# Performance work log

Hardware: AMD Instinct MI355X
Metric: run time of the kernel (lower is better)

Reference implementation:

```python
import jax, jax.numpy as jnp
import numpy as np

B, T, F, H, C = 128, 2048, 2, 64, 2
EPS = 1e-5  # BatchNorm eps (eval mode, running stats)


def setup_inputs() -> dict:
    key = jax.random.key(0)
    ks = jax.random.split(key, 23)
    rn = lambda k, s, sc=0.1: jax.random.normal(k, s, jnp.float32) * sc
    return {
        "x": jax.random.normal(ks[0], (B, T, F), jnp.float32),
        "tags": jax.random.randint(ks[1], (B, T), 0, C),
        "cw1": rn(ks[2], (H, F)), "cb1": rn(ks[3], (H,)),
        "cwr": rn(ks[4], (3, H, H)), "cbr": rn(ks[5], (3, H)),
        "bn_g": 1.0 + rn(ks[6], (4, H)), "bn_b": rn(ks[7], (4, H)),
        "bn_m": rn(ks[8], (4, H)),
        "bn_v": 0.5 + jax.random.uniform(ks[9], (4, H), jnp.float32),
        "wih_f": rn(ks[10], (4 * H, H)), "whh_f": rn(ks[11], (4 * H, H)),
        "bih_f": rn(ks[12], (4 * H,)), "bhh_f": rn(ks[13], (4 * H,)),
        "wih_b": rn(ks[14], (4 * H, H)), "whh_b": rn(ks[15], (4 * H, H)),
        "bih_b": rn(ks[16], (4 * H,)), "bhh_b": rn(ks[17], (4 * H,)),
        "fc_w": rn(ks[18], (C, 2 * H)), "fc_b": rn(ks[19], (C,)),
        "crf_start": rn(ks[20], (C,)), "crf_end": rn(ks[21], (C,)),
        "crf_trans": rn(ks[22], (C, C)),
    }


def _block(y, w, b, g, be, m, v):
    # Conv1d(kernel_size=1) == per-timestep linear; GELU (exact erf); eval BatchNorm1d
    y = jnp.einsum('bti,hi->bth', y, w) + b
    y = jax.nn.gelu(y, approximate=False)
    return (y - m) / jnp.sqrt(v + EPS) * g + be


def _lstm(xs, wih, whh, bih, bhh):
    # xs: [T, B, H]; PyTorch gate order i, f, g, o
    h0 = jnp.zeros((xs.shape[1], whh.shape[1]), xs.dtype)

    def step(carry, xt):
        h, c = carry
        z = xt @ wih.T + h @ whh.T + bih + bhh
        i, f, g, o = jnp.split(z, 4, axis=-1)
        c = jax.nn.sigmoid(f) * c + jax.nn.sigmoid(i) * jnp.tanh(g)
        h = jax.nn.sigmoid(o) * jnp.tanh(c)
        return (h, c), h

    _, hs = jax.lax.scan(step, (h0, h0), xs)
    return hs  # [T, B, H]


def reference(x, tags, cw1, cb1, cwr, cbr, bn_g, bn_b, bn_m, bn_v,
              wih_f, whh_f, bih_f, bhh_f, wih_b, whh_b, bih_b, bhh_b,
              fc_w, fc_b, crf_start, crf_end, crf_trans):
    # --- 1x1-conv stack (dropout is identity in eval) ---
    y = _block(x, cw1, cb1, bn_g[0], bn_b[0], bn_m[0], bn_v[0])
    for i in range(3):
        y = _block(y, cwr[i], cbr[i], bn_g[i + 1], bn_b[i + 1], bn_m[i + 1], bn_v[i + 1])
    # --- BiLSTM ---
    xt = jnp.transpose(y, (1, 0, 2))                       # [T, B, H]
    hf = _lstm(xt, wih_f, whh_f, bih_f, bhh_f)
    hb = _lstm(xt[::-1], wih_b, whh_b, bih_b, bhh_b)[::-1]
    h = jnp.concatenate([hf, hb], axis=-1)                 # [T, B, 2H]
    em = jnp.transpose(h @ fc_w.T + fc_b, (1, 0, 2))       # [B, T, C] emissions
    # --- CRF log-partition (forward algorithm, lax.scan over time) ---
    alpha0 = crf_start + em[:, 0]                          # [B, C]

    def step(alpha, et):
        a = jax.scipy.special.logsumexp(alpha[:, :, None] + crf_trans[None], axis=1) + et
        return a, None

    alpha, _ = jax.lax.scan(step, alpha0, jnp.transpose(em[:, 1:], (1, 0, 2)))
    logZ = jax.scipy.special.logsumexp(alpha + crf_end, axis=1)  # [B]
    # --- gold-path score ---
    num = crf_start[tags[:, 0]] + crf_end[tags[:, -1]]
    num = num + jnp.take_along_axis(em, tags[:, :, None], axis=2)[..., 0].sum(axis=1)
    num = num + crf_trans[tags[:, :-1], tags[:, 1:]].sum(axis=1)
    # model returns -crf(logits, tags) with reduction='sum' -> scalar NLL
    return -(num - logZ).sum()
```

## Files before the change

### kernel.cpp

```cpp
#include <hip/hip_runtime.h>
#include <hip/hip_bf16.h>

#define BB 128
#define TT 2048
#define HH 64
#define BT (BB * TT)
#define EPS_BN 1e-5f

typedef unsigned short ushort_t;
typedef short s8v __attribute__((ext_vector_type(8)));
typedef float f4v __attribute__((ext_vector_type(4)));

__device__ __forceinline__ float gelu_exact(float x) {
    return 0.5f * x * (1.0f + erff(x * 0.70710678118654752440f));
}
__device__ __forceinline__ ushort_t f2bf(float v) {
    __hip_bfloat16 h = __float2bfloat16(v);
    return *reinterpret_cast<ushort_t*>(&h);
}
__device__ __forceinline__ float lse2(float a, float b) {
    float m = fmaxf(a, b);
    return m + log1pf(__expf(-fabsf(a - b)));
}

__global__ __launch_bounds__(256, 4) void conv_kernel(
    const float* __restrict__ x, const float* __restrict__ cw1, const float* __restrict__ cb1,
    const float* __restrict__ cwr, const float* __restrict__ cbr,
    const float* __restrict__ bn_g, const float* __restrict__ bn_b,
    const float* __restrict__ bn_m, const float* __restrict__ bn_v,
    ushort_t* __restrict__ y) {
    __shared__ ushort_t s_wc[3 * 64 * 64];
    __shared__ float s_l1[64 * 4];
    __shared__ float s_sc[256], s_sh[256];
    __shared__ float s_cb[192];
    __shared__ ushort_t s_act[4][1024];

    int tid = threadIdx.x;
    for (int i = tid; i < 3 * 64 * 64; i += 256) {
        int row = (i >> 6) & 63, col = i & 63;
        unsigned by = (unsigned)((i >> 6) * 128 + col * 2) ^ (unsigned)((row & 7) << 4);
        s_wc[by >> 1] = f2bf(cwr[i]);
    }
    if (tid < 64) {
        s_l1[tid * 4 + 0] = cw1[tid * 2 + 0];
        s_l1[tid * 4 + 1] = cw1[tid * 2 + 1];
        s_l1[tid * 4 + 2] = cb1[tid];
    }
    if (tid < 256) {
        float sc = bn_g[tid] * rsqrtf(bn_v[tid] + EPS_BN);
        s_sc[tid] = sc;
        s_sh[tid] = bn_b[tid] - bn_m[tid] * sc;
    }
    if (tid < 192) s_cb[tid] = cbr[tid];
    __syncthreads();

    int wid = tid >> 6, l = tid & 63;
    int lrow = l & 15, lgrp = l >> 4;
    ushort_t* act = s_act[wid];
    int gwave = blockIdx.x * 4 + wid;

    for (int strip = gwave; strip < 16384; strip += 4096) {
        int p0 = strip << 4;
        float2 xv = ((const float2*)x)[p0 + lrow];
        s8v fa0, fa1;
#pragma unroll
        for (int j = 0; j < 8; ++j) {
            int c0 = lgrp * 8 + j, c1 = 32 + c0;
            float t0 = s_l1[c0 * 4] * xv.x + s_l1[c0 * 4 + 1] * xv.y + s_l1[c0 * 4 + 2];
            t0 = gelu_exact(t0) * s_sc[c0] + s_sh[c0];
            fa0[j] = (short)f2bf(t0);
            float t1 = s_l1[c1 * 4] * xv.x + s_l1[c1 * 4 + 1] * xv.y + s_l1[c1 * 4 + 2];
            t1 = gelu_exact(t1) * s_sc[c1] + s_sh[c1];
            fa1[j] = (short)f2bf(t1);
        }
#pragma unroll
        for (int L = 0; L < 3; ++L) {
            f4v acc[4];
#pragma unroll
            for (int nt = 0; nt < 4; ++nt) {
                acc[nt] = (f4v){0.f, 0.f, 0.f, 0.f};
                int row = nt * 16 + lrow;
                unsigned b0 = (unsigned)(L * 8192 + row * 128 + lgrp * 16) ^ (unsigned)((row & 7) << 4);
                unsigned b1 = (unsigned)(L * 8192 + row * 128 + lgrp * 16 + 64) ^ (unsigned)((row & 7) << 4);
                s8v fb0 = *(const s8v*)((const char*)s_wc + b0);
                s8v fb1 = *(const s8v*)((const char*)s_wc + b1);
                acc[nt] = __builtin_amdgcn_mfma_f32_16x16x32_bf16(fa0, fb0, acc[nt], 0, 0, 0);
                acc[nt] = __builtin_amdgcn_mfma_f32_16x16x32_bf16(fa1, fb1, acc[nt], 0, 0, 0);
            }
#pragma unroll
            for (int nt = 0; nt < 4; ++nt) {
                int ch = nt * 16 + lrow;
#pragma unroll
                for (int i = 0; i < 4; ++i) {
                    float v = acc[nt][i] + s_cb[L * 64 + ch];
                    v = gelu_exact(v) * s_sc[(L + 1) * 64 + ch] + s_sh[(L + 1) * 64 + ch];
                    int pos = lgrp * 4 + i;
                    unsigned by = (unsigned)(pos * 128 + ch * 2) ^ (unsigned)((pos & 7) << 4);
                    *(ushort_t*)((char*)act + by) = f2bf(v);
                }
            }
            if (L < 2) {
                unsigned r0 = (unsigned)(lrow * 128 + lgrp * 16) ^ (unsigned)((lrow & 7) << 4);
                unsigned r1 = (unsigned)(lrow * 128 + lgrp * 16 + 64) ^ (unsigned)((lrow & 7) << 4);
                fa0 = *(const s8v*)((const char*)act + r0);
                fa1 = *(const s8v*)((const char*)act + r1);
            }
        }
        int prow = l >> 2, pc = l & 3;
        unsigned so0 = (unsigned)(prow * 128 + pc * 32) ^ (unsigned)((prow & 7) << 4);
        unsigned so1 = (unsigned)(prow * 128 + pc * 32 + 16) ^ (unsigned)((prow & 7) << 4);
        s8v v0 = *(const s8v*)((const char*)act + so0);
        s8v v1 = *(const s8v*)((const char*)act + so1);
        char* yb = (char*)y + (size_t)(p0 + prow) * 128 + pc * 32;
        *(s8v*)yb = v0;
        *(s8v*)(yb + 16) = v1;
    }
}

__device__ __forceinline__ void em_emit(const float (*hist)[64], s8v femB0, s8v femB1,
                                        int lrow, int lgrp, float* __restrict__ em_ws,
                                        int dir, int b, int t_base, int dstep) {
    s8v fa0, fa1;
#pragma unroll
    for (int jj = 0; jj < 8; ++jj) {
        fa0[jj] = (short)f2bf(hist[lrow][lgrp * 8 + jj]);
        fa1[jj] = (short)f2bf(hist[lrow][32 + lgrp * 8 + jj]);
    }
    f4v acc = (f4v){0.f, 0.f, 0.f, 0.f};
    acc = __builtin_amdgcn_mfma_f32_16x16x32_bf16(fa0, femB0, acc, 0, 0, 0);
    acc = __builtin_amdgcn_mfma_f32_16x16x32_bf16(fa1, femB1, acc, 0, 0, 0);
    if (lrow < 2) {
#pragma unroll
        for (int i = 0; i < 4; ++i) {
            int s_loc = lgrp * 4 + i;
            int t = t_base + dstep * s_loc;
            em_ws[(((size_t)dir * TT + t) * BB + b) * 2 + lrow] = acc[i];
        }
    }
}

#define DOT4(g) (h0.x*wq[g][0].x + h0.y*wq[g][0].y + h0.z*wq[g][0].z + h0.w*wq[g][0].w \
               + h1.x*wq[g][1].x + h1.y*wq[g][1].y + h1.z*wq[g][1].z + h1.w*wq[g][1].w \
               + h2.x*wq[g][2].x + h2.y*wq[g][2].y + h2.z*wq[g][2].z + h2.w*wq[g][2].w \
               + h3.x*wq[g][3].x + h3.y*wq[g][3].y + h3.z*wq[g][3].z + h3.w*wq[g][3].w)

__global__ __launch_bounds__(256, 1) void lstm_kernel(
    const ushort_t* __restrict__ y,
    const float* __restrict__ whh_f, const float* __restrict__ whh_b,
    const float* __restrict__ wih_f, const float* __restrict__ wih_b,
    const float* __restrict__ bih_f, const float* __restrict__ bhh_f,
    const float* __restrict__ bih_b, const float* __restrict__ bhh_b,
    const float* __restrict__ fc_w, float* __restrict__ em_ws) {
    int blk = blockIdx.x;
    int dir = blk >> 7;
    int b = blk & 127;
    const float* whh = dir ? whh_b : whh_f;
    const float* wih = dir ? wih_b : wih_f;
    const float* bih = dir ? bih_b : bih_f;
    const float* bhh = dir ? bhh_b : bhh_f;

    int tid = threadIdx.x;
    int u = tid >> 2, kq = tid & 3;
    int wid = tid >> 6, l = tid & 63;
    int lrow = l & 15, lgrp = l >> 4;

    __shared__ ushort_t s_wih[256 * 64];
    __shared__ float s_pb[256];
    __shared__ float zbuf[16][256];
    __shared__ ushort_t s_y[16 * 64];
    __shared__ float hist[16][64];

    for (int i = tid; i < 256 * 64; i += 256) {
        int row = i >> 6, col = i & 63;
        unsigned by = (unsigned)(row * 128 + col * 2) ^ (unsigned)((row & 7) << 4);
        s_wih[by >> 1] = f2bf(wih[i]);
    }
    s_pb[tid] = bih[tid] + bhh[tid];
    if (tid < 64) hist[15][tid] = 0.f;

    float4 wq[4][4];
#pragma unroll
    for (int g = 0; g < 4; ++g)
#pragma unroll
        for (int m = 0; m < 4; ++m)
            wq[g][m] = *(const float4*)(whh + (size_t)(g * 64 + u) * 64 + kq * 16 + m * 4);

    s8v femB0 = {0, 0, 0, 0, 0, 0, 0, 0}, femB1 = {0, 0, 0, 0, 0, 0, 0, 0};
    if (wid == 0 && lrow < 2) {
#pragma unroll
        for (int jj = 0; jj < 8; ++jj) {
            int u0 = lgrp * 8 + jj;
            femB0[jj] = (short)f2bf(fc_w[lrow * 128 + dir * 64 + u0]);
            femB1[jj] = (short)f2bf(fc_w[lrow * 128 + dir * 64 + 32 + u0]);
        }
    }

    int t0 = dir ? (TT - 1) : 0;
    int dstep = dir ? -1 : 1;
    int m_st = tid >> 4, ch4 = tid & 15;
    const char* ybase = (const char*)y + (size_t)b * TT * 128;
    unsigned sy_by = (unsigned)(m_st * 128 + ch4 * 8) ^ (unsigned)((m_st & 7) << 4);
    uint2 yreg = *(const uint2*)(ybase + (size_t)(t0 + dstep * m_st) * 128 + ch4 * 8);

    __syncthreads();

    float c = 0.f;
    for (int strip = 0; strip < 128; ++strip) {
        *(uint2*)((char*)s_y + sy_by) = yreg;
        __syncthreads();
        {
            s8v fa0 = *(const s8v*)((const char*)s_y +
                        ((unsigned)(lrow * 128 + lgrp * 16) ^ (unsigned)((lrow & 7) << 4)));
            s8v fa1 = *(const s8v*)((const char*)s_y +
                        ((unsigned)(lrow * 128 + lgrp * 16 + 64) ^ (unsigned)((lrow & 7) << 4)));
#pragma unroll
            for (int nt = 0; nt < 4; ++nt) {
                int row = wid * 64 + nt * 16 + lrow;
                s8v fb0 = *(const s8v*)((const char*)s_wih +
                            ((unsigned)(row * 128 + lgrp * 16) ^ (unsigned)((row & 7) << 4)));
                s8v fb1 = *(const s8v*)((const char*)s_wih +
                            ((unsigned)(row * 128 + lgrp * 16 + 64) ^ (unsigned)((row & 7) << 4)));
                f4v acc = (f4v){0.f, 0.f, 0.f, 0.f};
                acc = __builtin_amdgcn_mfma_f32_16x16x32_bf16(fa0, fb0, acc, 0, 0, 0);
                acc = __builtin_amdgcn_mfma_f32_16x16x32_bf16(fa1, fb1, acc, 0, 0, 0);
                int u_ = nt * 16 + lrow;
                float bias = s_pb[row];
#pragma unroll
                for (int i = 0; i < 4; ++i) {
                    int pos = lgrp * 4 + i;
                    zbuf[pos][(u_ * 4 + wid) ^ lgrp] = acc[i] + bias;
                }
            }
            if (strip > 0 && wid == 0)
                em_emit(hist, femB0, femB1, lrow, lgrp, em_ws, dir, b,
                        t0 + dstep * ((strip - 1) * 16), dstep);
        }
        __syncthreads();
        float z_reg[16];
#pragma unroll
        for (int j = 0; j < 16; ++j) z_reg[j] = zbuf[j][tid ^ ((j >> 2) & 3)];
        if (strip + 1 < 128) {
            int tn = t0 + dstep * ((strip + 1) * 16 + m_st);
            yreg = *(const uint2*)(ybase + (size_t)tn * 128 + ch4 * 8);
        }
#pragma unroll
        for (int j = 0; j < 16; ++j) {
            int jm1 = (j + 15) & 15;
            const float4* hb4 = (const float4*)&hist[jm1][kq * 16];
            float4 h0 = hb4[0], h1 = hb4[1], h2 = hb4[2], h3 = hb4[3];
            float a0 = DOT4(0), a1 = DOT4(1), a2 = DOT4(2), a3 = DOT4(3);
            float zr = z_reg[j];
            a0 += (kq == 0) ? zr : 0.f;
            a1 += (kq == 1) ? zr : 0.f;
            a2 += (kq == 2) ? zr : 0.f;
            a3 += (kq == 3) ? zr : 0.f;
            a0 += __shfl_xor(a0, 1); a0 += __shfl_xor(a0, 2);
            a1 += __shfl_xor(a1, 1); a1 += __shfl_xor(a1, 2);
            a2 += __shfl_xor(a2, 1); a2 += __shfl_xor(a2, 2);
            a3 += __shfl_xor(a3, 1); a3 += __shfl_xor(a3, 2);
            float zg = (kq == 0) ? a0 : (kq == 1) ? a1 : (kq == 2) ? a2 : a3;
            float sgm = 1.f / (1.f + __expf((kq == 2) ? (-zg - zg) : -zg));
            float val = (kq == 2) ? (2.f * sgm - 1.f) : sgm;
            float v1 = __shfl_xor(val, 1), v2 = __shfl_xor(val, 2), v3 = __shfl_xor(val, 3);
            float gi = (kq == 0) ? val : (kq == 1) ? v1 : (kq == 2) ? v2 : v3;
            float gf = (kq == 1) ? val : (kq == 0) ? v1 : (kq == 3) ? v2 : v3;
            float gg = (kq == 2) ? val : (kq == 3) ? v1 : (kq == 0) ? v2 : v3;
            float go = (kq == 3) ? val : (kq == 2) ? v1 : (kq == 1) ? v2 : v3;
            c = gf * c + gi * gg;
            float e2 = __expf(2.f * c);
            float h = go * (1.f - 2.f / (e2 + 1.f));
            if (kq == 0) hist[j][u] = h;
            __syncthreads();
        }
    }
    if (wid == 0)
        em_emit(hist, femB0, femB1, lrow, lgrp, em_ws, dir, b,
                t0 + dstep * (127 * 16), dstep);
}

__global__ __launch_bounds__(128) void crf_kernel(
    const float* __restrict__ em_ws, const int* __restrict__ tags,
    const float* __restrict__ fc_b, const float* __restrict__ crf_start,
    const float* __restrict__ crf_end, const float* __restrict__ crf_trans,
    float* __restrict__ out) {
    int b = threadIdx.x;
    float fb0 = fc_b[0], fb1 = fc_b[1];
    float t00 = crf_trans[0], t01 = crf_trans[1], t10 = crf_trans[2], t11 = crf_trans[3];
    float s0 = crf_start[0], s1 = crf_start[1];
    float ee0 = crf_end[0], ee1 = crf_end[1];
    const float2* p0 = (const float2*)em_ws;
    const float2* p1 = p0 + (size_t)TT * BB;
    const int* tgp = tags + (size_t)b * TT;

    float2 ea = p0[b];
    float2 eb = p1[b];
    float e0 = ea.x + eb.x + fb0;
    float e1 = ea.y + eb.y + fb1;
    float a0 = s0 + e0, a1 = s1 + e1;
    int tp = tgp[0];
    float num = (tp ? s1 : s0) + (tp ? e1 : e0);

    int t = 1;
    for (; t + 8 <= TT; t += 8) {
        float2 ca[8], cb[8];
        int ct[8];
#pragma unroll
        for (int i = 0; i < 8; ++i) {
            ca[i] = p0[(size_t)(t + i) * BB + b];
            cb[i] = p1[(size_t)(t + i) * BB + b];
            ct[i] = tgp[t + i];
        }
#pragma unroll
        for (int i = 0; i < 8; ++i) {
            float f0 = ca[i].x + cb[i].x + fb0;
            float f1 = ca[i].y + cb[i].y + fb1;
            float n0 = lse2(a0 + t00, a1 + t10) + f0;
            float n1 = lse2(a0 + t01, a1 + t11) + f1;
            a0 = n0; a1 = n1;
            int tgi = ct[i];
            num += (tgi ? f1 : f0) + (tp ? (tgi ? t11 : t10) : (tgi ? t01 : t00));
            tp = tgi;
        }
    }
    for (; t < TT; ++t) {
        float2 ca = p0[(size_t)t * BB + b];
        float2 cb = p1[(size_t)t * BB + b];
        float f0 = ca.x + cb.x + fb0;
        float f1 = ca.y + cb.y + fb1;
        float n0 = lse2(a0 + t00, a1 + t10) + f0;
        float n1 = lse2(a0 + t01, a1 + t11) + f1;
        a0 = n0; a1 = n1;
        int tgi = tgp[t];
        num += (tgi ? f1 : f0) + (tp ? (tgi ? t11 : t10) : (tgi ? t01 : t00));
        tp = tgi;
    }
    num += tp ? ee1 : ee0;
    float logZ = lse2(a0 + ee0, a1 + ee1);
    float nll = logZ - num;
    __shared__ float red[BB];
    red[b] = nll;
    __syncthreads();
    if (b == 0) {
        float s = 0.f;
        for (int i = 0; i < BB; ++i) s += red[i];
        out[0] = s;
    }
}

extern "C" void kernel_launch(void* const* d_in, const int* in_sizes, int n_in,
                              void* d_out, int out_size, void* d_ws, size_t ws_size,
                              hipStream_t stream) {
    const float* x = (const float*)d_in[0];
    const int* tags = (const int*)d_in[1];
    const float* cw1 = (const float*)d_in[2];
    const float* cb1 = (const float*)d_in[3];
    const float* cwr = (const float*)d_in[4];
    const float* cbr = (const float*)d_in[5];
    const float* bn_g = (const float*)d_in[6];
    const float* bn_b = (const float*)d_in[7];
    const float* bn_m = (const float*)d_in[8];
    const float* bn_v = (const float*)d_in[9];
    const float* wih_f = (const float*)d_in[10];
    const float* whh_f = (const float*)d_in[11];
    const float* bih_f = (const float*)d_in[12];
    const float* bhh_f = (const float*)d_in[13];
    const float* wih_b = (const float*)d_in[14];
    const float* whh_b = (const float*)d_in[15];
    const float* bih_b = (const float*)d_in[16];
    const float* bhh_b = (const float*)d_in[17];
    const float* fc_w = (const float*)d_in[18];
    const float* fc_b = (const float*)d_in[19];
    const float* crf_start = (const float*)d_in[20];
    const float* crf_end = (const float*)d_in[21];
    const float* crf_trans = (const float*)d_in[22];
    float* out = (float*)d_out;

    ushort_t* y = (ushort_t*)d_ws;
    float* em = (float*)((char*)d_ws + (size_t)BT * 64 * 2);

    conv_kernel<<<1024, 256, 0, stream>>>(x, cw1, cb1, cwr, cbr, bn_g, bn_b, bn_m, bn_v, y);
    lstm_kernel<<<256, 256, 0, stream>>>(y, whh_f, whh_b, wih_f, wih_b,
                                         bih_f, bhh_f, bih_b, bhh_b, fc_w, em);
    crf_kernel<<<1, 128, 0, stream>>>(em, tags, fc_b, crf_start, crf_end, crf_trans, out);
}
```

Baseline: 2.232 ms.

## Batch LSTM recurrence over 16 sequences with MFMA and parallelize CRF over time

The LSTM moves from one block per (direction, batch) with scalar FP32 dot products to 16 blocks that each handle 16 batch rows. Both the recurrent h@Whh and the input projections now run as bf16 MFMA, with weights held in registers and h kept in a swizzled LDS ring. The CRF forward pass switches from one thread per batch scanning all 2048 steps to a time-parallel scheme: each thread builds a 2x2 log-semiring transfer product over 16 steps, and the products are then combined, with a separate sum kernel at the end. The trade-offs are fewer blocks (16 of the GPU's many CUs), bf16 rounding of h in the recurrence, and one extra kernel launch.

```diff
diff --git a/kernel.cpp b/kernel.cpp
--- a/kernel.cpp
+++ b/kernel.cpp
@@ -117,32 +117,87 @@
     }
 }
 
-__device__ __forceinline__ void em_emit(const float (*hist)[64], s8v femB0, s8v femB1,
-                                        int lrow, int lgrp, float* __restrict__ em_ws,
-                                        int dir, int b, int t_base, int dstep) {
-    s8v fa0, fa1;
-#pragma unroll
-    for (int jj = 0; jj < 8; ++jj) {
-        fa0[jj] = (short)f2bf(hist[lrow][lgrp * 8 + jj]);
-        fa1[jj] = (short)f2bf(hist[lrow][32 + lgrp * 8 + jj]);
-    }
-    f4v acc = (f4v){0.f, 0.f, 0.f, 0.f};
-    acc = __builtin_amdgcn_mfma_f32_16x16x32_bf16(fa0, femB0, acc, 0, 0, 0);
-    acc = __builtin_amdgcn_mfma_f32_16x16x32_bf16(fa1, femB1, acc, 0, 0, 0);
-    if (lrow < 2) {
+__device__ __forceinline__ unsigned ring_addr(int slot, int bb, int ub) {
+    return (unsigned)(slot * 2048) + (((unsigned)(bb * 128 + ub)) ^ ((unsigned)((bb & 7) << 4)));
+}
+
+template <int PAR>
+__device__ __forceinline__ void lstm_strip(
+    int s, int w, int lb, int lg, int b, int d, int t0, int dstep,
+    const s8v (&whhA)[4][2], const s8v (&wihA)[4][2],
+    const f4v (&zbias)[4], const s8v (&femA)[2],
+    const s8v (&ybCur)[4][2], s8v (&ybNxt)[4][2],
+    float (&cst)[4], ushort_t* ring,
+    const char* __restrict__ ybase, float2* __restrict__ emv) {
+    f4v zin[4][4];
+#pragma unroll
+    for (int g = 0; g < 4; ++g)
+#pragma unroll
+        for (int ct = 0; ct < 4; ++ct) {
+            f4v a = zbias[g];
+            a = __builtin_amdgcn_mfma_f32_16x16x32_bf16(wihA[g][0], ybCur[ct][0], a, 0, 0, 0);
+            a = __builtin_amdgcn_mfma_f32_16x16x32_bf16(wihA[g][1], ybCur[ct][1], a, 0, 0, 0);
+            zin[g][ct] = a;
+        }
+    if (s + 1 < 512) {
+#pragma unroll
+        for (int ct = 0; ct < 4; ++ct) {
+            int t = t0 + dstep * ((s + 1) * 4 + ct);
+            const char* p = ybase + (size_t)t * 128 + lg * 16;
+            ybNxt[ct][0] = *(const s8v*)p;
+            ybNxt[ct][1] = *(const s8v*)(p + 64);
+        }
+    }
+    if (w == 0 && s > 0) {
+#pragma unroll
+        for (int ct = 0; ct < 4; ++ct) {
+            int slot = (1 - PAR) * 4 + ct;
+            s8v hlo = *(const s8v*)((const char*)ring + ring_addr(slot, lb, lg * 16));
+            s8v hhi = *(const s8v*)((const char*)ring + ring_addr(slot, lb, 64 + lg * 16));
+            f4v a = (f4v){0.f, 0.f, 0.f, 0.f};
+            a = __builtin_amdgcn_mfma_f32_16x16x32_bf16(femA[0], hlo, a, 0, 0, 0);
+            a = __builtin_amdgcn_mfma_f32_16x16x32_bf16(femA[1], hhi, a, 0, 0, 0);
+            if (lg == 0) {
+                int t = t0 + dstep * ((s - 1) * 4 + ct);
+                emv[((size_t)d * TT + t) * BB + b] = make_float2(a[0], a[1]);
+            }
+        }
+    }
+#pragma unroll
+    for (int j = 0; j < 4; ++j) {
+        const int prev = (j == 0) ? ((1 - PAR) * 4 + 3) : (PAR * 4 + j - 1);
+        const int slot = PAR * 4 + j;
+        s8v hlo = *(const s8v*)((const char*)ring + ring_addr(prev, lb, lg * 16));
+        s8v hhi = *(const s8v*)((const char*)ring + ring_addr(prev, lb, 64 + lg * 16));
+        f4v a0 = __builtin_amdgcn_mfma_f32_16x16x32_bf16(whhA[0][0], hlo, zin[0][j], 0, 0, 0);
+        f4v a1 = __builtin_amdgcn_mfma_f32_16x16x32_bf16(whhA[1][0], hlo, zin[1][j], 0, 0, 0);
+        f4v a2 = __builtin_amdgcn_mfma_f32_16x16x32_bf16(whhA[2][0], hlo, zin[2][j], 0, 0, 0);
+        f4v a3 = __builtin_amdgcn_mfma_f32_16x16x32_bf16(whhA[3][0], hlo, zin[3][j], 0, 0, 0);
+        a0 = __builtin_amdgcn_mfma_f32_16x16x32_bf16(whhA[0][1], hhi, a0, 0, 0, 0);
+        a1 = __builtin_amdgcn_mfma_f32_16x16x32_bf16(whhA[1][1], hhi, a1, 0, 0, 0);
+        a2 = __builtin_amdgcn_mfma_f32_16x16x32_bf16(whhA[2][1], hhi, a2, 0, 0, 0);
+        a3 = __builtin_amdgcn_mfma_f32_16x16x32_bf16(whhA[3][1], hhi, a3, 0, 0, 0);
+        unsigned hp0 = 0, hp1 = 0;
 #pragma unroll
         for (int i = 0; i < 4; ++i) {
-            int s_loc = lgrp * 4 + i;
-            int t = t_base + dstep * s_loc;
-            em_ws[(((size_t)dir * TT + t) * BB + b) * 2 + lrow] = acc[i];
-        }
-    }
-}
-
-#define DOT4(g) (h0.x*wq[g][0].x + h0.y*wq[g][0].y + h0.z*wq[g][0].z + h0.w*wq[g][0].w \
-               + h1.x*wq[g][1].x + h1.y*wq[g][1].y + h1.z*wq[g][1].z + h1.w*wq[g][1].w \
-               + h2.x*wq[g][2].x + h2.y*wq[g][2].y + h2.z*wq[g][2].z + h2.w*wq[g][2].w \
-               + h3.x*wq[g][3].x + h3.y*wq[g][3].y + h3.z*wq[g][3].z + h3.w*wq[g][3].w)
+            float zi = a0[i], zf = a1[i], zg = a2[i], zo = a3[i];
+            float ig = 1.f / (1.f + __expf(-zi));
+            float fg = 1.f / (1.f + __expf(-zf));
+            float gg = 1.f - 2.f / (__expf(2.f * zg) + 1.f);
+            float og = 1.f / (1.f + __expf(-zo));
+            float cn = fg * cst[i] + ig * gg;
+            cst[i] = cn;
+            float th = 1.f - 2.f / (__expf(2.f * cn) + 1.f);
+            unsigned hb_ = (unsigned)f2bf(og * th);
+            if (i == 0) hp0 = hb_;
+            else if (i == 1) hp0 |= hb_ << 16;
+            else if (i == 2) hp1 = hb_;
+            else hp1 |= hb_ << 16;
+        }
+        *(uint2*)((char*)ring + ring_addr(slot, lb, (16 * w + lg * 4) * 2)) = make_uint2(hp0, hp1);
+        __syncthreads();
+    }
+}
 
 __global__ __launch_bounds__(256, 1) void lstm_kernel(
     const ushort_t* __restrict__ y,
@@ -151,196 +206,155 @@
     const float* __restrict__ bih_f, const float* __restrict__ bhh_f,
     const float* __restrict__ bih_b, const float* __restrict__ bhh_b,
     const float* __restrict__ fc_w, float* __restrict__ em_ws) {
-    int blk = blockIdx.x;
-    int dir = blk >> 7;
-    int b = blk & 127;
-    const float* whh = dir ? whh_b : whh_f;
-    const float* wih = dir ? wih_b : wih_f;
-    const float* bih = dir ? bih_b : bih_f;
-    const float* bhh = dir ? bhh_b : bhh_f;
-
+    __shared__ ushort_t ring[8 * 1024];
+    int d = blockIdx.x >> 3, bg = blockIdx.x & 7;
+    const float* whh = d ? whh_b : whh_f;
+    const float* wih = d ? wih_b : wih_f;
+    const float* bih = d ? bih_b : bih_f;
+    const float* bhh = d ? bhh_b : bhh_f;
     int tid = threadIdx.x;
-    int u = tid >> 2, kq = tid & 3;
-    int wid = tid >> 6, l = tid & 63;
-    int lrow = l & 15, lgrp = l >> 4;
-
-    __shared__ ushort_t s_wih[256 * 64];
-    __shared__ float s_pb[256];
-    __shared__ float zbuf[16][256];
-    __shared__ ushort_t s_y[16 * 64];
-    __shared__ float hist[16][64];
-
-    for (int i = tid; i < 256 * 64; i += 256) {
-        int row = i >> 6, col = i & 63;
-        unsigned by = (unsigned)(row * 128 + col * 2) ^ (unsigned)((row & 7) << 4);
-        s_wih[by >> 1] = f2bf(wih[i]);
-    }
-    s_pb[tid] = bih[tid] + bhh[tid];
-    if (tid < 64) hist[15][tid] = 0.f;
-
-    float4 wq[4][4];
+    int w = tid >> 6, l = tid & 63, lb = l & 15, lg = l >> 4;
+    int b = bg * 16 + lb;
+
+    for (int i = tid; i < 4096; i += 256) ((unsigned*)ring)[i] = 0u;
+
+    s8v whhA[4][2], wihA[4][2];
 #pragma unroll
     for (int g = 0; g < 4; ++g)
 #pragma unroll
-        for (int m = 0; m < 4; ++m)
-            wq[g][m] = *(const float4*)(whh + (size_t)(g * 64 + u) * 64 + kq * 16 + m * 4);
-
-    s8v femB0 = {0, 0, 0, 0, 0, 0, 0, 0}, femB1 = {0, 0, 0, 0, 0, 0, 0, 0};
-    if (wid == 0 && lrow < 2) {
-#pragma unroll
-        for (int jj = 0; jj < 8; ++jj) {
-            int u0 = lgrp * 8 + jj;
-            femB0[jj] = (short)f2bf(fc_w[lrow * 128 + dir * 64 + u0]);
-            femB1[jj] = (short)f2bf(fc_w[lrow * 128 + dir * 64 + 32 + u0]);
-        }
-    }
-
-    int t0 = dir ? (TT - 1) : 0;
-    int dstep = dir ? -1 : 1;
-    int m_st = tid >> 4, ch4 = tid & 15;
+        for (int kh = 0; kh < 2; ++kh) {
+            s8v va, vb;
+#pragma unroll
+            for (int j = 0; j < 8; ++j) {
+                int row = g * 64 + 16 * w + lb;
+                int k = kh * 32 + lg * 8 + j;
+                va[j] = (short)f2bf(whh[(size_t)row * 64 + k]);
+                vb[j] = (short)f2bf(wih[(size_t)row * 64 + k]);
+            }
+            whhA[g][kh] = va;
+            wihA[g][kh] = vb;
+        }
+    f4v zbias[4];
+#pragma unroll
+    for (int g = 0; g < 4; ++g)
+#pragma unroll
+        for (int i = 0; i < 4; ++i) {
+            int u = 16 * w + lg * 4 + i;
+            zbias[g][i] = bih[g * 64 + u] + bhh[g * 64 + u];
+        }
+    s8v femA[2];
+#pragma unroll
+    for (int kh = 0; kh < 2; ++kh)
+#pragma unroll
+        for (int j = 0; j < 8; ++j) {
+            int k = kh * 32 + lg * 8 + j;
+            femA[kh][j] = (lb < 2) ? (short)f2bf(fc_w[lb * 128 + d * 64 + k]) : (short)0;
+        }
+
+    int t0 = d ? (TT - 1) : 0;
+    int dstep = d ? -1 : 1;
     const char* ybase = (const char*)y + (size_t)b * TT * 128;
-    unsigned sy_by = (unsigned)(m_st * 128 + ch4 * 8) ^ (unsigned)((m_st & 7) << 4);
-    uint2 yreg = *(const uint2*)(ybase + (size_t)(t0 + dstep * m_st) * 128 + ch4 * 8);
-
+    float2* emv = (float2*)em_ws;
+
+    s8v ybA[4][2], ybB[4][2];
+#pragma unroll
+    for (int ct = 0; ct < 4; ++ct) {
+        int t = t0 + dstep * ct;
+        const char* p = ybase + (size_t)t * 128 + lg * 16;
+        ybA[ct][0] = *(const s8v*)p;
+        ybA[ct][1] = *(const s8v*)(p + 64);
+    }
+    float cst[4] = {0.f, 0.f, 0.f, 0.f};
     __syncthreads();
 
-    float c = 0.f;
-    for (int strip = 0; strip < 128; ++strip) {
-        *(uint2*)((char*)s_y + sy_by) = yreg;
-        __syncthreads();
-        {
-            s8v fa0 = *(const s8v*)((const char*)s_y +
-                        ((unsigned)(lrow * 128 + lgrp * 16) ^ (unsigned)((lrow & 7) << 4)));
-            s8v fa1 = *(const s8v*)((const char*)s_y +
-                        ((unsigned)(lrow * 128 + lgrp * 16 + 64) ^ (unsigned)((lrow & 7) << 4)));
-#pragma unroll
-            for (int nt = 0; nt < 4; ++nt) {
-                int row = wid * 64 + nt * 16 + lrow;
-                s8v fb0 = *(const s8v*)((const char*)s_wih +
-                            ((unsigned)(row * 128 + lgrp * 16) ^ (unsigned)((row & 7) << 4)));
-                s8v fb1 = *(const s8v*)((const char*)s_wih +
-                            ((unsigned)(row * 128 + lgrp * 16 + 64) ^ (unsigned)((row & 7) << 4)));
-                f4v acc = (f4v){0.f, 0.f, 0.f, 0.f};
-                acc = __builtin_amdgcn_mfma_f32_16x16x32_bf16(fa0, fb0, acc, 0, 0, 0);
-                acc = __builtin_amdgcn_mfma_f32_16x16x32_bf16(fa1, fb1, acc, 0, 0, 0);
-                int u_ = nt * 16 + lrow;
-                float bias = s_pb[row];
-#pragma unroll
-                for (int i = 0; i < 4; ++i) {
-                    int pos = lgrp * 4 + i;
-                    zbuf[pos][(u_ * 4 + wid) ^ lgrp] = acc[i] + bias;
-                }
-            }
-            if (strip > 0 && wid == 0)
-                em_emit(hist, femB0, femB1, lrow, lgrp, em_ws, dir, b,
-                        t0 + dstep * ((strip - 1) * 16), dstep);
-        }
-        __syncthreads();
-        float z_reg[16];
-#pragma unroll
-        for (int j = 0; j < 16; ++j) z_reg[j] = zbuf[j][tid ^ ((j >> 2) & 3)];
-        if (strip + 1 < 128) {
-            int tn = t0 + dstep * ((strip + 1) * 16 + m_st);
-            yreg = *(const uint2*)(ybase + (size_t)tn * 128 + ch4 * 8);
-        }
-#pragma unroll
-        for (int j = 0; j < 16; ++j) {
-            int jm1 = (j + 15) & 15;
-            const float4* hb4 = (const float4*)&hist[jm1][kq * 16];
-            float4 h0 = hb4[0], h1 = hb4[1], h2 = hb4[2], h3 = hb4[3];
-            float a0 = DOT4(0), a1 = DOT4(1), a2 = DOT4(2), a3 = DOT4(3);
-            float zr = z_reg[j];
-            a0 += (kq == 0) ? zr : 0.f;
-            a1 += (kq == 1) ? zr : 0.f;
-            a2 += (kq == 2) ? zr : 0.f;
-            a3 += (kq == 3) ? zr : 0.f;
-            a0 += __shfl_xor(a0, 1); a0 += __shfl_xor(a0, 2);
-            a1 += __shfl_xor(a1, 1); a1 += __shfl_xor(a1, 2);
-            a2 += __shfl_xor(a2, 1); a2 += __shfl_xor(a2, 2);
-            a3 += __shfl_xor(a3, 1); a3 += __shfl_xor(a3, 2);
-            float zg = (kq == 0) ? a0 : (kq == 1) ? a1 : (kq == 2) ? a2 : a3;
-            float sgm = 1.f / (1.f + __expf((kq == 2) ? (-zg - zg) : -zg));
-            float val = (kq == 2) ? (2.f * sgm - 1.f) : sgm;
-            float v1 = __shfl_xor(val, 1), v2 = __shfl_xor(val, 2), v3 = __shfl_xor(val, 3);
-            float gi = (kq == 0) ? val : (kq == 1) ? v1 : (kq == 2) ? v2 : v3;
-            float gf = (kq == 1) ? val : (kq == 0) ? v1 : (kq == 3) ? v2 : v3;
-            float gg = (kq == 2) ? val : (kq == 3) ? v1 : (kq == 0) ? v2 : v3;
-            float go = (kq == 3) ? val : (kq == 2) ? v1 : (kq == 1) ? v2 : v3;
-            c = gf * c + gi * gg;
-            float e2 = __expf(2.f * c);
-            float h = go * (1.f - 2.f / (e2 + 1.f));
-            if (kq == 0) hist[j][u] = h;
-            __syncthreads();
-        }
-    }
-    if (wid == 0)
-        em_emit(hist, femB0, femB1, lrow, lgrp, em_ws, dir, b,
-                t0 + dstep * (127 * 16), dstep);
+    for (int sp = 0; sp < 256; ++sp) {
+        lstm_strip<0>(2 * sp, w, lb, lg, b, d, t0, dstep, whhA, wihA, zbias, femA,
+                      ybA, ybB, cst, ring, ybase, emv);
+        lstm_strip<1>(2 * sp + 1, w, lb, lg, b, d, t0, dstep, whhA, wihA, zbias, femA,
+                      ybB, ybA, cst, ring, ybase, emv);
+    }
+    if (w == 0) {
+#pragma unroll
+        for (int ct = 0; ct < 4; ++ct) {
+            int slot = 4 + ct;
+            s8v hlo = *(const s8v*)((const char*)ring + ring_addr(slot, lb, lg * 16));
+            s8v hhi = *(const s8v*)((const char*)ring + ring_addr(slot, lb, 64 + lg * 16));
+            f4v a = (f4v){0.f, 0.f, 0.f, 0.f};
+            a = __builtin_amdgcn_mfma_f32_16x16x32_bf16(femA[0], hlo, a, 0, 0, 0);
+            a = __builtin_amdgcn_mfma_f32_16x16x32_bf16(femA[1], hhi, a, 0, 0, 0);
+            if (lg == 0) {
+                int t = t0 + dstep * (511 * 4 + ct);
+                emv[((size_t)d * TT + t) * BB + b] = make_float2(a[0], a[1]);
+            }
+        }
+    }
 }
 
 __global__ __launch_bounds__(128) void crf_kernel(
     const float* __restrict__ em_ws, const int* __restrict__ tags,
     const float* __restrict__ fc_b, const float* __restrict__ crf_start,
     const float* __restrict__ crf_end, const float* __restrict__ crf_trans,
-    float* __restrict__ out) {
-    int b = threadIdx.x;
+    float* __restrict__ nll_ws) {
+    int b = blockIdx.x, c = threadIdx.x;
     float fb0 = fc_b[0], fb1 = fc_b[1];
     float t00 = crf_trans[0], t01 = crf_trans[1], t10 = crf_trans[2], t11 = crf_trans[3];
-    float s0 = crf_start[0], s1 = crf_start[1];
-    float ee0 = crf_end[0], ee1 = crf_end[1];
     const float2* p0 = (const float2*)em_ws;
     const float2* p1 = p0 + (size_t)TT * BB;
-    const int* tgp = tags + (size_t)b * TT;
-
-    float2 ea = p0[b];
-    float2 eb = p1[b];
-    float e0 = ea.x + eb.x + fb0;
-    float e1 = ea.y + eb.y + fb1;
-    float a0 = s0 + e0, a1 = s1 + e1;
-    int tp = tgp[0];
-    float num = (tp ? s1 : s0) + (tp ? e1 : e0);
-
-    int t = 1;
-    for (; t + 8 <= TT; t += 8) {
-        float2 ca[8], cb[8];
-        int ct[8];
-#pragma unroll
-        for (int i = 0; i < 8; ++i) {
-            ca[i] = p0[(size_t)(t + i) * BB + b];
-            cb[i] = p1[(size_t)(t + i) * BB + b];
-            ct[i] = tgp[t + i];
-        }
-#pragma unroll
-        for (int i = 0; i < 8; ++i) {
-            float f0 = ca[i].x + cb[i].x + fb0;
-            float f1 = ca[i].y + cb[i].y + fb1;
-            float n0 = lse2(a0 + t00, a1 + t10) + f0;
-            float n1 = lse2(a0 + t01, a1 + t11) + f1;
-            a0 = n0; a1 = n1;
-            int tgi = ct[i];
-            num += (tgi ? f1 : f0) + (tp ? (tgi ? t11 : t10) : (tgi ? t01 : t00));
-            tp = tgi;
-        }
-    }
-    for (; t < TT; ++t) {
-        float2 ca = p0[(size_t)t * BB + b];
-        float2 cb = p1[(size_t)t * BB + b];
-        float f0 = ca.x + cb.x + fb0;
-        float f1 = ca.y + cb.y + fb1;
-        float n0 = lse2(a0 + t00, a1 + t10) + f0;
-        float n1 = lse2(a0 + t01, a1 + t11) + f1;
-        a0 = n0; a1 = n1;
-        int tgi = tgp[t];
-        num += (tgi ? f1 : f0) + (tp ? (tgi ? t11 : t10) : (tgi ? t01 : t00));
-        tp = tgi;
-    }
-    num += tp ? ee1 : ee0;
-    float logZ = lse2(a0 + ee0, a1 + ee1);
-    float nll = logZ - num;
+    const int* tg = tags + (size_t)b * TT;
+
+    int tbeg = 1 + 16 * c;
+    int tend = min(TT, tbeg + 16);
+    float P00, P01, P10, P11;
+    float np = 0.f;
+    int tprev = tg[tbeg - 1];
+    {
+        float2 ea = p0[(size_t)tbeg * BB + b], eb = p1[(size_t)tbeg * BB + b];
+        float e0 = ea.x + eb.x + fb0, e1 = ea.y + eb.y + fb1;
+        P00 = t00 + e0; P01 = t01 + e1; P10 = t10 + e0; P11 = t11 + e1;
+        int tc = tg[tbeg];
+        np += (tc ? e1 : e0) + (tprev ? (tc ? t11 : t10) : (tc ? t01 : t00));
+        tprev = tc;
+    }
+    for (int t = tbeg + 1; t < tend; ++t) {
+        float2 ea = p0[(size_t)t * BB + b], eb = p1[(size_t)t * BB + b];
+        float e0 = ea.x + eb.x + fb0, e1 = ea.y + eb.y + fb1;
+        float n00 = lse2(P00 + t00, P01 + t10) + e0;
+        float n01 = lse2(P00 + t01, P01 + t11) + e1;
+        float n10 = lse2(P10 + t00, P11 + t10) + e0;
+        float n11 = lse2(P10 + t01, P11 + t11) + e1;
+        P00 = n00; P01 = n01; P10 = n10; P11 = n11;
+        int tc = tg[t];
+        np += (tc ? e1 : e0) + (tprev ? (tc ? t11 : t10) : (tc ? t01 : t00));
+        tprev = tc;
+    }
+    __shared__ float sP[128][4];
+    __shared__ float sN[128];
+    sP[c][0] = P00; sP[c][1] = P01; sP[c][2] = P10; sP[c][3] = P11;
+    sN[c] = np;
+    __syncthreads();
+    if (c == 0) {
+        float2 ea = p0[b], eb = p1[b];
+        float e0 = ea.x + eb.x + fb0, e1 = ea.y + eb.y + fb1;
+        float a0 = crf_start[0] + e0, a1 = crf_start[1] + e1;
+        float num = tg[0] ? (crf_start[1] + e1) : (crf_start[0] + e0);
+        for (int k = 0; k < 128; ++k) {
+            float q0 = lse2(a0 + sP[k][0], a1 + sP[k][2]);
+            float q1 = lse2(a0 + sP[k][1], a1 + sP[k][3]);
+            a0 = q0; a1 = q1;
+            num += sN[k];
+        }
+        num += crf_end[tg[TT - 1]];
+        float logZ = lse2(a0 + crf_end[0], a1 + crf_end[1]);
+        nll_ws[b] = logZ - num;
+    }
+}
+
+__global__ __launch_bounds__(128) void sum_kernel(const float* __restrict__ nll_ws,
+                                                  float* __restrict__ out) {
     __shared__ float red[BB];
-    red[b] = nll;
+    red[threadIdx.x] = nll_ws[threadIdx.x];
     __syncthreads();
-    if (b == 0) {
+    if (threadIdx.x == 0) {
         float s = 0.f;
         for (int i = 0; i < BB; ++i) s += red[i];
         out[0] = s;
@@ -377,9 +391,11 @@
 
     ushort_t* y = (ushort_t*)d_ws;
     float* em = (float*)((char*)d_ws + (size_t)BT * 64 * 2);
+    float* nll = (float*)((char*)d_ws + (size_t)BT * 64 * 2 + (size_t)2 * TT * BB * 2 * 4);
 
     conv_kernel<<<1024, 256, 0, stream>>>(x, cw1, cb1, cwr, cbr, bn_g, bn_b, bn_m, bn_v, y);
-    lstm_kernel<<<256, 256, 0, stream>>>(y, whh_f, whh_b, wih_f, wih_b,
-                                         bih_f, bhh_f, bih_b, bhh_b, fc_w, em);
-    crf_kernel<<<1, 128, 0, stream>>>(em, tags, fc_b, crf_start, crf_end, crf_trans, out);
-}
+    lstm_kernel<<<16, 256, 0, stream>>>(y, whh_f, whh_b, wih_f, wih_b,
+                                        bih_f, bhh_f, bih_b, bhh_b, fc_w, em);
+    crf_kernel<<<128, 128, 0, stream>>>(em, tags, fc_b, crf_start, crf_end, crf_trans, nll);
+    sum_kernel<<<1, 128, 0, stream>>>(nll, out);
+}
```

Result: no change. 2.199 ms (-1.5%).
